# Optimization experiments

Hardware: AMD Instinct MI355X
Metric: run time of the kernel (lower is better)

## Reference

```python
import jax, jax.numpy as jnp
import numpy as np

B, S, DIM = 2, 8192, 1024
NH, NKV, HD = 16, 4, 64
GROUPS = NH // NKV
CHUNK = 128
THETA = 10000.0


def _slopes(h):
    # ALiBi-style per-head decay slopes (h is a power of two)
    return jnp.asarray([2.0 ** (-8.0 / h * (i + 1)) for i in range(h)], dtype=jnp.float32)


def _rope_tables(s, d):
    inv = 1.0 / (THETA ** (np.arange(0, d, 2, dtype=np.float64) / d))
    freqs = np.outer(np.arange(s, dtype=np.float64), inv)  # [s, d/2]
    emb = np.concatenate([freqs, freqs], axis=-1)  # [s, d]
    return jnp.asarray(np.cos(emb), jnp.float32), jnp.asarray(np.sin(emb), jnp.float32)


def _apply_rope(x, cos, sin):
    # x: [b, h, s, d]; cos/sin: [s, d]
    x1, x2 = jnp.split(x, 2, axis=-1)
    rot = jnp.concatenate([-x2, x1], axis=-1)
    return x * cos + rot * sin


def _lightning_attn(q, k, v, slopes, chunk):
    # out[t] = sum_{i<=t} exp(-slope*(t-i)) * (q_t . k_i) * v_i, chunked O(n) recurrence
    b, h, s, d = q.shape
    nc = s // chunk
    t = jnp.arange(chunk, dtype=jnp.float32)
    sl = slopes[:, None, None]  # [h,1,1]
    mask = jnp.where(t[:, None] >= t[None, :],
                     jnp.exp(-sl * (t[:, None] - t[None, :])), 0.0)  # [h,C,C]
    q_dec = jnp.exp(-slopes[:, None] * (t + 1.0))[..., None]          # [h,C,1]
    k_dec = jnp.exp(-slopes[:, None] * (chunk - 1.0 - t))[..., None]  # [h,C,1]
    blk_dec = jnp.exp(-slopes * chunk)[None, :, None, None]           # [1,h,1,1]

    def to_chunks(x):
        return x.reshape(b, h, nc, chunk, d).transpose(2, 0, 1, 3, 4)  # [nc,b,h,C,d]

    qc, kc, vc = to_chunks(q), to_chunks(k), to_chunks(v)

    def step(kv, inp):
        qi, ki, vi = inp  # [b,h,C,d]
        scores = jnp.einsum('bhtd,bhsd->bhts', qi, ki) * mask
        o = jnp.einsum('bhts,bhsd->bhtd', scores, vi) \
            + jnp.einsum('bhtd,bhde->bhte', qi * q_dec, kv)
        kv = blk_dec * kv + jnp.einsum('bhtd,bhte->bhde', ki * k_dec, vi)
        return kv, o

    kv0 = jnp.zeros((b, h, d, d), q.dtype)
    _, outs = jax.lax.scan(step, kv0, (qc, kc, vc))  # outs: [nc,b,h,C,d]
    return outs.transpose(1, 2, 0, 3, 4).reshape(b, h, s, d)


def setup_inputs() -> dict:
    key = jax.random.key(0)
    k0, k1, k2, k3, k4 = jax.random.split(key, 5)
    x = jax.random.normal(k0, (B, S, DIM), jnp.float32)
    Wq = jax.random.normal(k1, (NH * HD, DIM), jnp.float32) * 0.02
    Wk = jax.random.normal(k2, (NKV * HD, DIM), jnp.float32) * 0.02
    Wv = jax.random.normal(k3, (NKV * HD, DIM), jnp.float32) * 0.02
    Wo = jax.random.normal(k4, (DIM, NH * HD), jnp.float32) * 0.02
    return {"x": x, "Wq": Wq, "Wk": Wk, "Wv": Wv, "Wo": Wo}


def reference(x, Wq, Wk, Wv, Wo):
    b, s, _ = x.shape
    q = (x @ Wq.T).reshape(b, s, NH, HD).transpose(0, 2, 1, 3)
    k = (x @ Wk.T).reshape(b, s, NKV, HD).transpose(0, 2, 1, 3)
    v = (x @ Wv.T).reshape(b, s, NKV, HD).transpose(0, 2, 1, 3)
    cos, sin = _rope_tables(s, HD)
    q = _apply_rope(q, cos, sin)
    k = _apply_rope(k, cos, sin)
    # GQA expand: head index = kv_head*groups + g  <=>  repeat along head axis
    k = jnp.repeat(k, GROUPS, axis=1)
    v = jnp.repeat(v, GROUPS, axis=1)
    out = _lightning_attn(q, k, v, _slopes(NH), CHUNK)  # [b,NH,s,HD]
    out = out.transpose(0, 2, 1, 3).reshape(b, s, NH * HD)
    return out @ Wo.T
```

## Files before the change

### kernel.cpp

```cpp
#include <hip/hip_runtime.h>
#include <hip/hip_bf16.h>

#define B_ 2
#define S_ 8192
#define DIM_ 1024
#define NH_ 16
#define NKV_ 4
#define HD_ 64
#define NC_ 64

typedef __bf16 bf16x8 __attribute__((ext_vector_type(8)));
typedef float f32x4 __attribute__((ext_vector_type(4)));
using bf16 = __hip_bfloat16;

#define ASYNC16(gp, lp) __builtin_amdgcn_global_load_lds( \
    (__attribute__((address_space(1))) void*)(void*)(gp), \
    (__attribute__((address_space(3))) void*)(void*)(lp), 16, 0, 0)

__global__ __launch_bounds__(256) void prep_kernel(const float* __restrict__ x, const float* __restrict__ Wq,
                                                   const float* __restrict__ Wk, const float* __restrict__ Wv,
                                                   const float* __restrict__ Wo, bf16* __restrict__ xb,
                                                   bf16* __restrict__ wqkv, bf16* __restrict__ wo,
                                                   float* __restrict__ cosd, float* __restrict__ sind) {
    int bid = blockIdx.x;
    if (bid < 16384) {
        size_t i = ((size_t)bid * 256 + threadIdx.x) * 4;
        const float4 f = *(const float4*)(x + i);
        bf16 t[4];
        t[0] = __float2bfloat16(f.x); t[1] = __float2bfloat16(f.y);
        t[2] = __float2bfloat16(f.z); t[3] = __float2bfloat16(f.w);
        *(uint2*)(xb + i) = *(const uint2*)t;
    } else if (bid < 18944) {
        size_t e = ((size_t)(bid - 16384) * 256 + threadIdx.x) * 4;
        const float* src;
        bf16* dst;
        if (e < 1048576)        { src = Wq + e;             dst = wqkv + e; }
        else if (e < 1310720)   { src = Wk + (e - 1048576); dst = wqkv + e; }
        else if (e < 1572864)   { src = Wv + (e - 1310720); dst = wqkv + e; }
        else                    { src = Wo + (e - 1572864); dst = wo + (e - 1572864); }
        const float4 f = *(const float4*)src;
        bf16 t[4];
        t[0] = __float2bfloat16(f.x); t[1] = __float2bfloat16(f.y);
        t[2] = __float2bfloat16(f.z); t[3] = __float2bfloat16(f.w);
        *(uint2*)dst = *(const uint2*)t;
    } else {
        int idx = (bid - 18944) * 256 + threadIdx.x;
        int s = idx >> 5, i = idx & 31;
        double inv = exp((double)i * (-9.210340371976184 / 32.0));
        double rev = ((double)s * inv) * 0.15915494309189535;
        double frac = rev - floor(rev);
        float a = (float)frac * 6.2831853071795865f;
        cosd[idx] = __cosf(a);
        sind[idx] = __sinf(a);
    }
}

template <typename OT>
__global__ __launch_bounds__(256, 3) void gemm_bt_kernel(const bf16* __restrict__ A, const bf16* __restrict__ Bm,
                                                         OT* __restrict__ C, int M, int N, int K, int rope_ncols,
                                                         const float* __restrict__ cosd,
                                                         const float* __restrict__ sind) {
    __shared__ bf16 As[128 * 64];
    __shared__ bf16 Bs[128 * 64];
    const int tid = threadIdx.x;
    const int bm = blockIdx.x * 128, bn = blockIdx.y * 128;
    const int wave = tid >> 6, lane = tid & 63;
    const int wm = (wave >> 1) * 64, wn = (wave & 1) * 64;
    const int lr = lane & 15, quad = lane >> 4;
    const int srow = wave * 32;
    const int lrow = lane >> 3;
    const int lchunk = ((lane & 7) ^ lrow) * 8;
    const bf16* Ag = A + (size_t)(bm + srow + lrow) * K + lchunk;
    const bf16* Bg = Bm + (size_t)(bn + srow + lrow) * K + lchunk;
    f32x4 acc[4][4] = {};
    for (int k0 = 0; k0 < K; k0 += 64) {
#pragma unroll
        for (int p = 0; p < 4; ++p) {
            ASYNC16(Ag + (size_t)(p * 8) * K + k0, &As[(srow + p * 8) * 64]);
            ASYNC16(Bg + (size_t)(p * 8) * K + k0, &Bs[(srow + p * 8) * 64]);
        }
        __syncthreads();
#pragma unroll
        for (int kk = 0; kk < 64; kk += 32) {
            const int sw = (((kk >> 3) + quad) ^ (lr & 7)) << 3;
            bf16x8 af[4], bfr[4];
#pragma unroll
            for (int i = 0; i < 4; ++i) af[i] = *(const bf16x8*)(&As[(wm + i * 16 + lr) * 64 + sw]);
#pragma unroll
            for (int i = 0; i < 4; ++i) bfr[i] = *(const bf16x8*)(&Bs[(wn + i * 16 + lr) * 64 + sw]);
#pragma unroll
            for (int mi = 0; mi < 4; ++mi)
#pragma unroll
                for (int ni = 0; ni < 4; ++ni)
                    acc[mi][ni] = __builtin_amdgcn_mfma_f32_16x16x32_bf16(af[mi], bfr[ni], acc[mi][ni], 0, 0, 0);
        }
        __syncthreads();
    }
    if (bn + wn < rope_ncols) {
#pragma unroll
        for (int mi = 0; mi < 4; ++mi)
#pragma unroll
            for (int r = 0; r < 4; ++r) {
                int row = bm + wm + mi * 16 + quad * 4 + r;
                int s = row & (S_ - 1);
#pragma unroll
                for (int ni = 0; ni < 2; ++ni) {
                    int i = ni * 16 + lr;
                    float cs = cosd[(s << 5) + i];
                    float sn = sind[(s << 5) + i];
                    float x1 = acc[mi][ni][r], x2 = acc[mi][ni + 2][r];
                    acc[mi][ni][r] = x1 * cs - x2 * sn;
                    acc[mi][ni + 2][r] = x2 * cs + x1 * sn;
                }
            }
    }
#pragma unroll
    for (int mi = 0; mi < 4; ++mi)
#pragma unroll
        for (int ni = 0; ni < 4; ++ni)
#pragma unroll
            for (int r = 0; r < 4; ++r) {
                int row = bm + wm + mi * 16 + quad * 4 + r;
                int col = bn + wn + ni * 16 + lr;
                float v = acc[mi][ni][r];
                if constexpr (__is_same(OT, float)) C[(size_t)row * N + col] = v;
                else C[(size_t)row * N + col] = __float2bfloat16(v);
            }
}


__global__ __launch_bounds__(256, 4) void chunk_kv_kernel(const bf16* __restrict__ qkv, bf16* __restrict__ Cout) {
    const int j = blockIdx.x, h = blockIdx.y, b = blockIdx.z;
    const int g = h >> 2;
    const float slope = exp2f(-0.5f * (float)(h + 1));
    __shared__ bf16 kdT[64 * 136];
    __shared__ bf16 vT[64 * 136];
    const int tid = threadIdx.x;
#pragma unroll
    for (int p = 0; p < 4; ++p) {
        int flat = p * 256 + tid;
        int t = flat >> 3, d0 = (flat & 7) * 8;
        const size_t row = (size_t)(b * S_ + j * 128 + t);
        uint4 kw = *(const uint4*)(qkv + row * 1536 + 1024 + g * 64 + d0);
        uint4 vw = *(const uint4*)(qkv + row * 1536 + 1280 + g * 64 + d0);
        float kdec = __expf(-slope * (float)(127 - t));
        const bf16* kp = (const bf16*)&kw;
        const bf16* vp = (const bf16*)&vw;
#pragma unroll
        for (int i = 0; i < 8; ++i) {
            int e = d0 + i;
            int sw = (((t >> 3) & ~7) << 3) + ((((t >> 3) ^ (e >> 3)) & 7) << 3) + (t & 7);
            kdT[e * 136 + sw] = __float2bfloat16(__bfloat162float(kp[i]) * kdec);
            vT[e * 136 + sw] = vp[i];
        }
    }
    __syncthreads();
    const int wave = tid >> 6, lane = tid & 63, lr = lane & 15, quad = lane >> 4;
    const int ew = wave * 16;
    f32x4 acc[4] = {};
#pragma unroll
    for (int ks = 0; ks < 128; ks += 32) {
        int qa = (ks >> 3) + quad;
        int qhi = (qa & ~7) << 3;
        int ea = ew + lr;
        bf16x8 a = *(const bf16x8*)(&vT[ea * 136 + qhi + (((qa ^ (ea >> 3)) & 7) << 3)]);
#pragma unroll
        for (int ni = 0; ni < 4; ++ni) {
            int eb = ni * 16 + lr;
            bf16x8 bb = *(const bf16x8*)(&kdT[eb * 136 + qhi + (((qa ^ (eb >> 3)) & 7) << 3)]);
            acc[ni] = __builtin_amdgcn_mfma_f32_16x16x32_bf16(a, bb, acc[ni], 0, 0, 0);
        }
    }
    bf16* out = Cout + ((size_t)((b * NH_ + h) * NC_ + j)) * 4096;
#pragma unroll
    for (int ni = 0; ni < 4; ++ni)
#pragma unroll
        for (int r = 0; r < 4; ++r)
            out[(ew + quad * 4 + r) * 64 + ni * 16 + lr] = __float2bfloat16(acc[ni][r]);
}

__global__ __launch_bounds__(256) void scan_kv_kernel(const bf16* __restrict__ Cin, bf16* __restrict__ st) {
    const int bh = blockIdx.x >> 4;
    const int f = ((blockIdx.x & 15) << 8) + threadIdx.x;
    const int h = bh & (NH_ - 1);
    const float slope = exp2f(-0.5f * (float)(h + 1));
    const float bdec = __expf(-slope * 128.0f);
    const bf16* Cb = Cin + (size_t)bh * NC_ * 4096 + f;
    bf16* sb = st + (size_t)bh * NC_ * 4096 + f;
    float carry = 0.f;
#pragma unroll 8
    for (int c = 0; c < NC_; ++c) {
        sb[(size_t)c * 4096] = __float2bfloat16(carry);
        carry = bdec * carry + __bfloat162float(Cb[(size_t)c * 4096]);
    }
}

__global__ __launch_bounds__(256, 3) void attn_chunk_kernel(const bf16* __restrict__ qkv,
                                                            const bf16* __restrict__ kvst,
                                                            bf16* __restrict__ outb) {
    const int c = blockIdx.x, h = blockIdx.y, b = blockIdx.z;
    const int g = h >> 2;
    const float slope = exp2f(-0.5f * (float)(h + 1));
    __shared__ bf16 smem[26112];
    bf16* qs  = smem;
    bf16* kbs = smem + 9216;
    bf16* Ps  = smem;
    bf16* vT  = smem + 17408;
    const int tid = threadIdx.x;
    const int wave = tid >> 6, lane = tid & 63, lr = lane & 15, quad = lane >> 4;
#pragma unroll
    for (int p = 0; p < 4; ++p) {
        int flat = p * 256 + tid;
        int t = flat >> 3, d0 = (flat & 7) * 8;
        size_t row = (size_t)(b * S_ + c * 128 + t);
        *(uint4*)(&qs[t * 72 + d0]) = *(const uint4*)(qkv + row * 1536 + h * 64 + d0);
        *(uint4*)(&kbs[t * 72 + d0]) = *(const uint4*)(qkv + row * 1536 + 1024 + g * 64 + d0);
    }
    __syncthreads();
    const int m0 = wave * 32;
    f32x4 sacc[2][8] = {};
#pragma unroll
    for (int kk = 0; kk < 64; kk += 32) {
        bf16x8 af0 = *(const bf16x8*)(&qs[(m0 + lr) * 72 + kk + quad * 8]);
        bf16x8 af1 = *(const bf16x8*)(&qs[(m0 + 16 + lr) * 72 + kk + quad * 8]);
#pragma unroll
        for (int ni = 0; ni < 8; ++ni) {
            bf16x8 bfr = *(const bf16x8*)(&kbs[(ni * 16 + lr) * 72 + kk + quad * 8]);
            sacc[0][ni] = __builtin_amdgcn_mfma_f32_16x16x32_bf16(af0, bfr, sacc[0][ni], 0, 0, 0);
            sacc[1][ni] = __builtin_amdgcn_mfma_f32_16x16x32_bf16(af1, bfr, sacc[1][ni], 0, 0, 0);
        }
    }
    f32x4 oacc[2][4] = {};
    const bf16* kvb = kvst + ((size_t)((b * NH_ + h) * NC_ + c)) * 4096;
    float qd0 = __expf(-slope * (float)(m0 + lr + 1));
    float qd1 = __expf(-slope * (float)(m0 + 16 + lr + 1));
#pragma unroll
    for (int kk = 0; kk < 64; kk += 32) {
        bf16x8 a0 = *(const bf16x8*)(&qs[(m0 + lr) * 72 + kk + quad * 8]);
        bf16x8 a1 = *(const bf16x8*)(&qs[(m0 + 16 + lr) * 72 + kk + quad * 8]);
#pragma unroll
        for (int i = 0; i < 8; ++i) {
            a0[i] = (__bf16)((float)a0[i] * qd0);
            a1[i] = (__bf16)((float)a1[i] * qd1);
        }
#pragma unroll
        for (int ni = 0; ni < 4; ++ni) {
            bf16x8 bk = *(const bf16x8*)(kvb + (ni * 16 + lr) * 64 + kk + quad * 8);
            oacc[0][ni] = __builtin_amdgcn_mfma_f32_16x16x32_bf16(a0, bk, oacc[0][ni], 0, 0, 0);
            oacc[1][ni] = __builtin_amdgcn_mfma_f32_16x16x32_bf16(a1, bk, oacc[1][ni], 0, 0, 0);
        }
    }
    __syncthreads();
    float ftv[2][4], gtv[8];
#pragma unroll
    for (int mi = 0; mi < 2; ++mi)
#pragma unroll
        for (int r = 0; r < 4; ++r) ftv[mi][r] = __expf(-slope * (float)(mi * 16 + quad * 4 + r));
#pragma unroll
    for (int ni = 0; ni < 8; ++ni)
        gtv[ni] = __expf(-slope * fmaxf((float)(m0 - (ni * 16 + lr)), -31.0f));
#pragma unroll
    for (int mi = 0; mi < 2; ++mi)
#pragma unroll
        for (int ni = 0; ni < 8; ++ni)
#pragma unroll
            for (int r = 0; r < 4; ++r) {
                int t = m0 + mi * 16 + quad * 4 + r;
                int tp = ni * 16 + lr;
                float val = (t >= tp) ? sacc[mi][ni][r] * ftv[mi][r] * gtv[ni] : 0.f;
                int sw = (((tp >> 3) & ~7) << 3) + ((((tp >> 3) ^ (t >> 3)) & 7) << 3) + (tp & 7);
                Ps[t * 136 + sw] = __float2bfloat16(val);
            }
#pragma unroll
    for (int p = 0; p < 4; ++p) {
        int flat = p * 256 + tid;
        int t = flat >> 3, d0 = (flat & 7) * 8;
        size_t row = (size_t)(b * S_ + c * 128 + t);
        uint4 vw = *(const uint4*)(qkv + row * 1536 + 1280 + g * 64 + d0);
        const bf16* vp = (const bf16*)&vw;
#pragma unroll
        for (int i = 0; i < 8; ++i) {
            int e = d0 + i;
            int sw = (((t >> 3) & ~7) << 3) + ((((t >> 3) ^ (e >> 3)) & 7) << 3) + (t & 7);
            vT[e * 136 + sw] = vp[i];
        }
    }
    __syncthreads();
#pragma unroll
    for (int ks2 = 0; ks2 < 128; ks2 += 32) {
        int qa = (ks2 >> 3) + quad;
        int qhi = (qa & ~7) << 3;
        int ra0 = m0 + lr, ra1 = m0 + 16 + lr;
        bf16x8 af0 = *(const bf16x8*)(&Ps[ra0 * 136 + qhi + (((qa ^ (ra0 >> 3)) & 7) << 3)]);
        bf16x8 af1 = *(const bf16x8*)(&Ps[ra1 * 136 + qhi + (((qa ^ (ra1 >> 3)) & 7) << 3)]);
#pragma unroll
        for (int ni = 0; ni < 4; ++ni) {
            int eb = ni * 16 + lr;
            bf16x8 bfv = *(const bf16x8*)(&vT[eb * 136 + qhi + (((qa ^ (eb >> 3)) & 7) << 3)]);
            oacc[0][ni] = __builtin_amdgcn_mfma_f32_16x16x32_bf16(af0, bfv, oacc[0][ni], 0, 0, 0);
            oacc[1][ni] = __builtin_amdgcn_mfma_f32_16x16x32_bf16(af1, bfv, oacc[1][ni], 0, 0, 0);
        }
    }
#pragma unroll
    for (int mi = 0; mi < 2; ++mi)
#pragma unroll
        for (int ni = 0; ni < 4; ++ni)
#pragma unroll
            for (int r = 0; r < 4; ++r) {
                int t = m0 + mi * 16 + quad * 4 + r;
                int e = ni * 16 + lr;
                size_t row = (size_t)(b * S_ + c * 128 + t);
                outb[row * (NH_ * 64) + h * 64 + e] = __float2bfloat16(oacc[mi][ni][r]);
            }
}

extern "C" void kernel_launch(void* const* d_in, const int* in_sizes, int n_in,
                              void* d_out, int out_size, void* d_ws, size_t ws_size,
                              hipStream_t stream) {
    (void)in_sizes; (void)n_in; (void)out_size; (void)ws_size;
    const float* x  = (const float*)d_in[0];
    const float* Wq = (const float*)d_in[1];
    const float* Wk = (const float*)d_in[2];
    const float* Wv = (const float*)d_in[3];
    const float* Wo = (const float*)d_in[4];
    float* out = (float*)d_out;
    char* ws = (char*)d_ws;
    bf16*  xb    = (bf16*)(ws);
    bf16*  qkvb  = (bf16*)(ws + 33554432);
    bf16*  wqkvb = (bf16*)(ws + 83886080);
    bf16*  wob   = (bf16*)(ws + 87031808);
    float* cosd  = (float*)(ws + 89128960);
    float* sind  = (float*)(ws + 90177536);
    bf16*  Cbuf  = (bf16*)(ws + 91226112);
    bf16*  kvst  = (bf16*)(ws + 108003328);
    bf16*  attn  = xb;

    prep_kernel<<<19968, 256, 0, stream>>>(x, Wq, Wk, Wv, Wo, xb, wqkvb, wob, cosd, sind);

    gemm_bt_kernel<bf16><<<dim3(128, 12), 256, 0, stream>>>(xb, wqkvb, qkvb, 16384, 1536, 1024, 1280, cosd, sind);

    chunk_kv_kernel<<<dim3(NC_, NH_, B_), 256, 0, stream>>>(qkvb, Cbuf);
    scan_kv_kernel<<<512, 256, 0, stream>>>(Cbuf, kvst);
    attn_chunk_kernel<<<dim3(NC_, NH_, B_), 256, 0, stream>>>(qkvb, kvst, attn);

    gemm_bt_kernel<float><<<dim3(128, 8), 256, 0, stream>>>(attn, wob, out, 16384, 1024, 1024, 0, cosd, sind);
}
```

Measured before the change: 271.7 us.

## Replace projection GEMMs with 256x256 double-buffered, interleaved-prefetch GEMM kernel

Measured after the change: 274.0 us. Within noise of the previous version (+0.8%).

```diff
diff --git a/kernel.cpp b/kernel.cpp
--- a/kernel.cpp
+++ b/kernel.cpp
@@ -56,58 +56,106 @@
 }
 
 template <typename OT>
-__global__ __launch_bounds__(256, 3) void gemm_bt_kernel(const bf16* __restrict__ A, const bf16* __restrict__ Bm,
-                                                         OT* __restrict__ C, int M, int N, int K, int rope_ncols,
+__global__ __launch_bounds__(512, 1) void gemm256_kernel(const bf16* __restrict__ A, const bf16* __restrict__ Bm,
+                                                         OT* __restrict__ C, int N, int rope_ncols,
                                                          const float* __restrict__ cosd,
                                                          const float* __restrict__ sind) {
-    __shared__ bf16 As[128 * 64];
-    __shared__ bf16 Bs[128 * 64];
+    __shared__ bf16 As[2][16384];
+    __shared__ bf16 Bs[2][16384];
     const int tid = threadIdx.x;
-    const int bm = blockIdx.x * 128, bn = blockIdx.y * 128;
     const int wave = tid >> 6, lane = tid & 63;
-    const int wm = (wave >> 1) * 64, wn = (wave & 1) * 64;
+    const int wr = wave >> 2, wc = wave & 3;
+    const int wm = wr * 128, wn = wc * 64;
     const int lr = lane & 15, quad = lane >> 4;
-    const int srow = wave * 32;
-    const int lrow = lane >> 3;
-    const int lchunk = ((lane & 7) ^ lrow) * 8;
-    const bf16* Ag = A + (size_t)(bm + srow + lrow) * K + lchunk;
-    const bf16* Bg = Bm + (size_t)(bn + srow + lrow) * K + lchunk;
-    f32x4 acc[4][4] = {};
-    for (int k0 = 0; k0 < K; k0 += 64) {
-#pragma unroll
-        for (int p = 0; p < 4; ++p) {
-            ASYNC16(Ag + (size_t)(p * 8) * K + k0, &As[(srow + p * 8) * 64]);
-            ASYNC16(Bg + (size_t)(p * 8) * K + k0, &Bs[(srow + p * 8) * 64]);
-        }
-        __syncthreads();
-#pragma unroll
-        for (int kk = 0; kk < 64; kk += 32) {
-            const int sw = (((kk >> 3) + quad) ^ (lr & 7)) << 3;
-            bf16x8 af[4], bfr[4];
-#pragma unroll
-            for (int i = 0; i < 4; ++i) af[i] = *(const bf16x8*)(&As[(wm + i * 16 + lr) * 64 + sw]);
-#pragma unroll
-            for (int i = 0; i < 4; ++i) bfr[i] = *(const bf16x8*)(&Bs[(wn + i * 16 + lr) * 64 + sw]);
-#pragma unroll
-            for (int mi = 0; mi < 4; ++mi)
-#pragma unroll
-                for (int ni = 0; ni < 4; ++ni)
-                    acc[mi][ni] = __builtin_amdgcn_mfma_f32_16x16x32_bf16(af[mi], bfr[ni], acc[mi][ni], 0, 0, 0);
-        }
-        __syncthreads();
-    }
+    const int bm = blockIdx.x * 256, bn = blockIdx.y * 256;
+    const int sub0 = wave * 2, sub1 = sub0 + 1;
+    const int rr = lane >> 3;
+    const int cc = ((lane & 7) ^ rr) * 8;
+    const bf16* Ab = A + (size_t)(bm + rr) * 1024 + cc;
+    const bf16* Bb = Bm + (size_t)(bn + rr) * 1024 + cc;
+
+#define STG(dst, base, half, k0)                                                                        \
+    do {                                                                                                \
+        ASYNC16((base) + (size_t)((half) * 128 + sub0 * 8) * 1024 + (k0), &(dst)[(half) * 8192 + sub0 * 512]); \
+        ASYNC16((base) + (size_t)((half) * 128 + sub1 * 8) * 1024 + (k0), &(dst)[(half) * 8192 + sub1 * 512]); \
+    } while (0)
+
+#define RD_A(c, mbase)                                                                                  \
+    do {                                                                                                \
+        _Pragma("unroll") for (int mi_ = 0; mi_ < 4; ++mi_)                                             \
+            _Pragma("unroll") for (int kx_ = 0; kx_ < 2; ++kx_)                                         \
+                af[mi_][kx_] = *(const bf16x8*)&As[c][(wm + (mbase) + mi_ * 16 + lr) * 64 +              \
+                                                     ((kx_ * 4 + quad) ^ (lr & 7)) * 8];                \
+    } while (0)
+
+#define RD_B2(c, n0)                                                                                    \
+    do {                                                                                                \
+        _Pragma("unroll") for (int ni_ = 0; ni_ < 2; ++ni_)                                             \
+            _Pragma("unroll") for (int kx_ = 0; kx_ < 2; ++kx_)                                         \
+                bfr[(n0) + ni_][kx_] = *(const bf16x8*)&Bs[c][(wn + ((n0) + ni_) * 16 + lr) * 64 +      \
+                                                              ((kx_ * 4 + quad) ^ (lr & 7)) * 8];       \
+    } while (0)
+
+#define MM(mo, n0)                                                                                      \
+    do {                                                                                                \
+        __builtin_amdgcn_s_setprio(1);                                                                  \
+        _Pragma("unroll") for (int kx_ = 0; kx_ < 2; ++kx_)                                             \
+            _Pragma("unroll") for (int mi_ = 0; mi_ < 4; ++mi_)                                         \
+                _Pragma("unroll") for (int ni_ = 0; ni_ < 2; ++ni_)                                     \
+                    acc[(mo) + mi_][(n0) + ni_] = __builtin_amdgcn_mfma_f32_16x16x32_bf16(              \
+                        af[mi_][kx_], bfr[(n0) + ni_][kx_], acc[(mo) + mi_][(n0) + ni_], 0, 0, 0);      \
+        __builtin_amdgcn_s_setprio(0);                                                                  \
+    } while (0)
+
+#define BAR()                                                                                           \
+    do {                                                                                                \
+        __builtin_amdgcn_s_barrier();                                                                   \
+        __builtin_amdgcn_sched_barrier(0);                                                              \
+    } while (0)
+
+#define GQ_ITER(K1, K2, K3, LAST)                                                                       \
+    do {                                                                                                \
+         RD_A(0, 0); RD_B2(0, 0); STG(As[1], Ab, 0, (K1)); BAR(); MM(0, 0); BAR();              \
+         RD_B2(0, 2); STG(As[1], Ab, 1, (K1)); BAR(); MM(0, 2); BAR();                          \
+         RD_A(0, 64); if (!(LAST)) { STG(Bs[0], Bb, 0, (K2)); } BAR(); MM(4, 0); BAR();         \
+         if (!(LAST)) { STG(As[0], Ab, 0, (K2)); asm volatile("s_waitcnt vmcnt(4)"); }          \
+                 else { asm volatile("s_waitcnt vmcnt(0)"); }                                           \
+                 __builtin_amdgcn_sched_barrier(0); BAR(); MM(4, 2); BAR();                             \
+         RD_A(1, 0); RD_B2(1, 0); if (!(LAST)) { STG(As[0], Ab, 1, (K2)); } BAR(); MM(0, 0); BAR(); \
+         RD_B2(1, 2); if (!(LAST)) { STG(Bs[0], Bb, 1, (K2)); } BAR(); MM(0, 2); BAR();         \
+         RD_A(1, 64); if (!(LAST)) { STG(Bs[1], Bb, 0, (K3)); } BAR(); MM(4, 0); BAR();         \
+         if (!(LAST)) { STG(Bs[1], Bb, 1, (K3)); asm volatile("s_waitcnt vmcnt(4)");            \
+                                __builtin_amdgcn_sched_barrier(0); }                                    \
+                 BAR(); MM(4, 2); BAR();                                                                \
+    } while (0)
+
+    f32x4 acc[8][4] = {};
+    bf16x8 af[4][2];
+    bf16x8 bfr[4][2];
+
+    STG(Bs[0], Bb, 0, 0); STG(As[0], Ab, 0, 0); STG(As[0], Ab, 1, 0); STG(Bs[0], Bb, 1, 0);
+    STG(Bs[1], Bb, 0, 64); STG(Bs[1], Bb, 1, 64);
+    asm volatile("s_waitcnt vmcnt(4)");
+    __builtin_amdgcn_sched_barrier(0);
+    __builtin_amdgcn_s_barrier();
+
+    for (int i = 0; i < 7; ++i) {
+        GQ_ITER(i * 128 + 64, i * 128 + 128, i * 128 + 192, 0);
+    }
+    GQ_ITER(960, 0, 0, 1);
+
     if (bn + wn < rope_ncols) {
 #pragma unroll
-        for (int mi = 0; mi < 4; ++mi)
+        for (int mi = 0; mi < 8; ++mi)
 #pragma unroll
             for (int r = 0; r < 4; ++r) {
                 int row = bm + wm + mi * 16 + quad * 4 + r;
                 int s = row & (S_ - 1);
 #pragma unroll
                 for (int ni = 0; ni < 2; ++ni) {
-                    int i = ni * 16 + lr;
-                    float cs = cosd[(s << 5) + i];
-                    float sn = sind[(s << 5) + i];
+                    int ii = ni * 16 + lr;
+                    float cs = cosd[(s << 5) + ii];
+                    float sn = sind[(s << 5) + ii];
                     float x1 = acc[mi][ni][r], x2 = acc[mi][ni + 2][r];
                     acc[mi][ni][r] = x1 * cs - x2 * sn;
                     acc[mi][ni + 2][r] = x2 * cs + x1 * sn;
@@ -115,7 +163,7 @@
             }
     }
 #pragma unroll
-    for (int mi = 0; mi < 4; ++mi)
+    for (int mi = 0; mi < 8; ++mi)
 #pragma unroll
         for (int ni = 0; ni < 4; ++ni)
 #pragma unroll
@@ -126,6 +174,12 @@
                 if constexpr (__is_same(OT, float)) C[(size_t)row * N + col] = v;
                 else C[(size_t)row * N + col] = __float2bfloat16(v);
             }
+#undef STG
+#undef RD_A
+#undef RD_B2
+#undef MM
+#undef BAR
+#undef GQ_ITER
 }
 
 
@@ -337,11 +391,11 @@
 
     prep_kernel<<<19968, 256, 0, stream>>>(x, Wq, Wk, Wv, Wo, xb, wqkvb, wob, cosd, sind);
 
-    gemm_bt_kernel<bf16><<<dim3(128, 12), 256, 0, stream>>>(xb, wqkvb, qkvb, 16384, 1536, 1024, 1280, cosd, sind);
+    gemm256_kernel<bf16><<<dim3(64, 6), 512, 0, stream>>>(xb, wqkvb, qkvb, 1536, 1280, cosd, sind);
 
     chunk_kv_kernel<<<dim3(NC_, NH_, B_), 256, 0, stream>>>(qkvb, Cbuf);
     scan_kv_kernel<<<512, 256, 0, stream>>>(Cbuf, kvst);
     attn_chunk_kernel<<<dim3(NC_, NH_, B_), 256, 0, stream>>>(qkvb, kvst, attn);
 
-    gemm_bt_kernel<float><<<dim3(128, 8), 256, 0, stream>>>(attn, wob, out, 16384, 1024, 1024, 0, cosd, sind);
-}
+    gemm256_kernel<float><<<dim3(64, 4), 512, 0, stream>>>(attn, wob, out, 1024, 0, cosd, sind);
+}
```

## Share KV-head tiles across query heads in chunk_kv and async-load swizzled Q/K

Applied to the files above, without the earlier changes.

After: 264.1 us, median of 2. 2.8% less time.

```diff
diff --git a/kernel.cpp b/kernel.cpp
--- a/kernel.cpp
+++ b/kernel.cpp
@@ -129,54 +129,75 @@
 }
 
 
-__global__ __launch_bounds__(256, 4) void chunk_kv_kernel(const bf16* __restrict__ qkv, bf16* __restrict__ Cout) {
-    const int j = blockIdx.x, h = blockIdx.y, b = blockIdx.z;
-    const int g = h >> 2;
-    const float slope = exp2f(-0.5f * (float)(h + 1));
-    __shared__ bf16 kdT[64 * 136];
+__global__ __launch_bounds__(512) void chunk_kv_kernel(const bf16* __restrict__ qkv, bf16* __restrict__ Cout) {
+    const int j = blockIdx.x, g = blockIdx.y, b = blockIdx.z;
+    __shared__ bf16 kT[64 * 136];
     __shared__ bf16 vT[64 * 136];
     const int tid = threadIdx.x;
 #pragma unroll
-    for (int p = 0; p < 4; ++p) {
-        int flat = p * 256 + tid;
+    for (int p = 0; p < 2; ++p) {
+        int flat = p * 512 + tid;
         int t = flat >> 3, d0 = (flat & 7) * 8;
         const size_t row = (size_t)(b * S_ + j * 128 + t);
         uint4 kw = *(const uint4*)(qkv + row * 1536 + 1024 + g * 64 + d0);
         uint4 vw = *(const uint4*)(qkv + row * 1536 + 1280 + g * 64 + d0);
-        float kdec = __expf(-slope * (float)(127 - t));
         const bf16* kp = (const bf16*)&kw;
         const bf16* vp = (const bf16*)&vw;
 #pragma unroll
         for (int i = 0; i < 8; ++i) {
             int e = d0 + i;
             int sw = (((t >> 3) & ~7) << 3) + ((((t >> 3) ^ (e >> 3)) & 7) << 3) + (t & 7);
-            kdT[e * 136 + sw] = __float2bfloat16(__bfloat162float(kp[i]) * kdec);
+            kT[e * 136 + sw] = kp[i];
             vT[e * 136 + sw] = vp[i];
         }
     }
     __syncthreads();
     const int wave = tid >> 6, lane = tid & 63, lr = lane & 15, quad = lane >> 4;
-    const int ew = wave * 16;
-    f32x4 acc[4] = {};
+    const int eblk = (wave & 3) * 16;
+    const int hp = (wave >> 2) * 2;
+    f32x4 acc[2][4] = {};
+    float slope[2], g1[2];
+#pragma unroll
+    for (int hh = 0; hh < 2; ++hh) {
+        slope[hh] = exp2f(-0.5f * (float)(g * 4 + hp + hh + 1));
+        g1[hh] = __expf(slope[hh]);
+    }
 #pragma unroll
     for (int ks = 0; ks < 128; ks += 32) {
         int qa = (ks >> 3) + quad;
         int qhi = (qa & ~7) << 3;
-        int ea = ew + lr;
+        int ea = eblk + lr;
         bf16x8 a = *(const bf16x8*)(&vT[ea * 136 + qhi + (((qa ^ (ea >> 3)) & 7) << 3)]);
+        float av[8];
+#pragma unroll
+        for (int i = 0; i < 8; ++i) av[i] = (float)a[i];
+        bf16x8 bb[4];
 #pragma unroll
         for (int ni = 0; ni < 4; ++ni) {
             int eb = ni * 16 + lr;
-            bf16x8 bb = *(const bf16x8*)(&kdT[eb * 136 + qhi + (((qa ^ (eb >> 3)) & 7) << 3)]);
-            acc[ni] = __builtin_amdgcn_mfma_f32_16x16x32_bf16(a, bb, acc[ni], 0, 0, 0);
-        }
-    }
-    bf16* out = Cout + ((size_t)((b * NH_ + h) * NC_ + j)) * 4096;
-#pragma unroll
-    for (int ni = 0; ni < 4; ++ni)
-#pragma unroll
-        for (int r = 0; r < 4; ++r)
-            out[(ew + quad * 4 + r) * 64 + ni * 16 + lr] = __float2bfloat16(acc[ni][r]);
+            bb[ni] = *(const bf16x8*)(&kT[eb * 136 + qhi + (((qa ^ (eb >> 3)) & 7) << 3)]);
+        }
+#pragma unroll
+        for (int hh = 0; hh < 2; ++hh) {
+            float m = __expf(-slope[hh] * (float)(127 - ks - quad * 8));
+            bf16x8 as;
+#pragma unroll
+            for (int i = 0; i < 8; ++i) { as[i] = (__bf16)(av[i] * m); m *= g1[hh]; }
+#pragma unroll
+            for (int ni = 0; ni < 4; ++ni)
+                acc[hh][ni] = __builtin_amdgcn_mfma_f32_16x16x32_bf16(as, bb[ni], acc[hh][ni], 0, 0, 0);
+        }
+    }
+#pragma unroll
+    for (int hh = 0; hh < 2; ++hh) {
+        int h = g * 4 + hp + hh;
+        bf16* out = Cout + ((size_t)((b * NH_ + h) * NC_ + j)) * 4096;
+#pragma unroll
+        for (int ni = 0; ni < 4; ++ni)
+#pragma unroll
+            for (int r = 0; r < 4; ++r)
+                out[(eblk + quad * 4 + r) * 64 + ni * 16 + lr] = __float2bfloat16(acc[hh][ni][r]);
+    }
 }
 
 __global__ __launch_bounds__(256) void scan_kv_kernel(const bf16* __restrict__ Cin, bf16* __restrict__ st) {
@@ -203,29 +224,32 @@
     const float slope = exp2f(-0.5f * (float)(h + 1));
     __shared__ bf16 smem[26112];
     bf16* qs  = smem;
-    bf16* kbs = smem + 9216;
+    bf16* kbs = smem + 8192;
     bf16* Ps  = smem;
     bf16* vT  = smem + 17408;
     const int tid = threadIdx.x;
     const int wave = tid >> 6, lane = tid & 63, lr = lane & 15, quad = lane >> 4;
+    const int srow = lane >> 3;
+    const int schunk = ((lane & 7) ^ srow) * 8;
 #pragma unroll
     for (int p = 0; p < 4; ++p) {
-        int flat = p * 256 + tid;
-        int t = flat >> 3, d0 = (flat & 7) * 8;
-        size_t row = (size_t)(b * S_ + c * 128 + t);
-        *(uint4*)(&qs[t * 72 + d0]) = *(const uint4*)(qkv + row * 1536 + h * 64 + d0);
-        *(uint4*)(&kbs[t * 72 + d0]) = *(const uint4*)(qkv + row * 1536 + 1024 + g * 64 + d0);
-    }
+        int t0 = wave * 8 + p * 32;
+        size_t row = (size_t)(b * S_ + c * 128 + t0 + srow);
+        ASYNC16(qkv + row * 1536 + h * 64 + schunk, &qs[t0 * 64]);
+        ASYNC16(qkv + row * 1536 + 1024 + g * 64 + schunk, &kbs[t0 * 64]);
+    }
+    asm volatile("s_waitcnt vmcnt(0)");
     __syncthreads();
     const int m0 = wave * 32;
     f32x4 sacc[2][8] = {};
 #pragma unroll
     for (int kk = 0; kk < 64; kk += 32) {
-        bf16x8 af0 = *(const bf16x8*)(&qs[(m0 + lr) * 72 + kk + quad * 8]);
-        bf16x8 af1 = *(const bf16x8*)(&qs[(m0 + 16 + lr) * 72 + kk + quad * 8]);
+        const int sw = ((((kk >> 3) + quad) ^ (lr & 7)) & 7) << 3;
+        bf16x8 af0 = *(const bf16x8*)(&qs[(m0 + lr) * 64 + sw]);
+        bf16x8 af1 = *(const bf16x8*)(&qs[(m0 + 16 + lr) * 64 + sw]);
 #pragma unroll
         for (int ni = 0; ni < 8; ++ni) {
-            bf16x8 bfr = *(const bf16x8*)(&kbs[(ni * 16 + lr) * 72 + kk + quad * 8]);
+            bf16x8 bfr = *(const bf16x8*)(&kbs[(ni * 16 + lr) * 64 + sw]);
             sacc[0][ni] = __builtin_amdgcn_mfma_f32_16x16x32_bf16(af0, bfr, sacc[0][ni], 0, 0, 0);
             sacc[1][ni] = __builtin_amdgcn_mfma_f32_16x16x32_bf16(af1, bfr, sacc[1][ni], 0, 0, 0);
         }
@@ -236,8 +260,9 @@
     float qd1 = __expf(-slope * (float)(m0 + 16 + lr + 1));
 #pragma unroll
     for (int kk = 0; kk < 64; kk += 32) {
-        bf16x8 a0 = *(const bf16x8*)(&qs[(m0 + lr) * 72 + kk + quad * 8]);
-        bf16x8 a1 = *(const bf16x8*)(&qs[(m0 + 16 + lr) * 72 + kk + quad * 8]);
+        const int sw = ((((kk >> 3) + quad) ^ (lr & 7)) & 7) << 3;
+        bf16x8 a0 = *(const bf16x8*)(&qs[(m0 + lr) * 64 + sw]);
+        bf16x8 a1 = *(const bf16x8*)(&qs[(m0 + 16 + lr) * 64 + sw]);
 #pragma unroll
         for (int i = 0; i < 8; ++i) {
             a0[i] = (__bf16)((float)a0[i] * qd0);
@@ -339,7 +364,7 @@
 
     gemm_bt_kernel<bf16><<<dim3(128, 12), 256, 0, stream>>>(xb, wqkvb, qkvb, 16384, 1536, 1024, 1280, cosd, sind);
 
-    chunk_kv_kernel<<<dim3(NC_, NH_, B_), 256, 0, stream>>>(qkvb, Cbuf);
+    chunk_kv_kernel<<<dim3(NC_, NKV_, B_), 512, 0, stream>>>(qkvb, Cbuf);
     scan_kv_kernel<<<512, 256, 0, stream>>>(Cbuf, kvst);
     attn_chunk_kernel<<<dim3(NC_, NH_, B_), 256, 0, stream>>>(qkvb, kvst, attn);
 
```
